# Optimization experiments

Measured on AMD Instinct MI355X. Metric: run time of the kernel, lower is better.

The kernel has to match this reference:

```python
import jax, jax.numpy as jnp
import numpy as np

T, B, D, H = 512, 64, 512, 512  # seq_len, batch, input_size, hidden_size


def setup_inputs() -> dict:
    key = jax.random.key(0)
    ks = jax.random.split(key, 7)
    s = 1.0 / np.sqrt(H)
    return {
        "input": jax.random.normal(ks[0], (T, B, D), dtype=jnp.float32),
        "h0": jax.random.normal(ks[1], (B, H), dtype=jnp.float32),
        "c0": jax.random.normal(ks[2], (B, H), dtype=jnp.float32),
        "W_ih": jax.random.normal(ks[3], (4 * H, D), dtype=jnp.float32) * s,
        "W_hh": jax.random.normal(ks[4], (4 * H, H), dtype=jnp.float32) * s,
        "b_ih": jax.random.normal(ks[5], (4 * H,), dtype=jnp.float32) * s,
        "b_hh": jax.random.normal(ks[6], (4 * H,), dtype=jnp.float32) * s,
        "batch_first": 0,
    }


def reference(input, h0, c0, W_ih, W_hh, b_ih, b_hh, batch_first):
    # Dense (non-packed) branch of RNNLayer.forward with an LSTM cell.
    x = jnp.swapaxes(input, 0, 1) if batch_first else input  # [T, B, D]
    # Input projection is independent of the recurrence: precompute for all t.
    x_proj = jnp.einsum('tbd,gd->tbg', x, W_ih) + b_ih  # [T, B, 4H]

    def step(carry, xt):
        h, c = carry
        gates = xt + h @ W_hh.T + b_hh  # [B, 4H]
        i, f, g, o = jnp.split(gates, 4, axis=-1)
        c_new = jax.nn.sigmoid(f) * c + jax.nn.sigmoid(i) * jnp.tanh(g)
        h_new = jax.nn.sigmoid(o) * jnp.tanh(c_new)
        return (h_new, c_new), h_new

    (hT, cT), ys = jax.lax.scan(step, (h0, c0), x_proj)  # ys: [T, B, H]
    outputs = jnp.swapaxes(ys, 0, 1) if batch_first else ys
    return outputs, hT, cT
```

## Files before the change

### kernel.cpp

```cpp
#include <hip/hip_runtime.h>

typedef __attribute__((ext_vector_type(8))) short bfrag;
typedef __attribute__((ext_vector_type(4))) float f32x4;
typedef __attribute__((ext_vector_type(4))) int i32x4;

#define NT 512
#define NB 64
#define KD 512
#define NG 2048
#define GB 4
#define GH 16

#define YS_SZ (NT * NB * KD)
#define HT_OFF YS_SZ
#define CT_OFF (YS_SZ + NB * KD)

#define MB_BLK_WORDS 4096
#define MB_PAR_WORDS (GB * MB_BLK_WORDS)
#define MB_BYTES (2 * MB_PAR_WORDS * 8)

__device__ __forceinline__ unsigned short f2bf(float f) {
  unsigned u = __float_as_uint(f);
  u += 0x7fffu + ((u >> 16) & 1u);
  return (unsigned short)(u >> 16);
}
__device__ __forceinline__ float bf2f(unsigned short h) {
  return __uint_as_float(((unsigned)h) << 16);
}
__device__ __forceinline__ float sigm(float v) { return 1.f / (1.f + __expf(-v)); }
__device__ __forceinline__ float tanh_f(float v) { return 1.f - 2.f / (__expf(2.f * v) + 1.f); }

__global__ __launch_bounds__(256) void cvt_bf16(const float* __restrict__ src,
                                                unsigned short* __restrict__ dst, int n8) {
  int i = blockIdx.x * 256 + threadIdx.x;
  if (i >= n8) return;
  const float4 a = *(const float4*)(src + (size_t)i * 8);
  const float4 b = *(const float4*)(src + (size_t)i * 8 + 4);
  i32x4 v;
  v.x = (int)(f2bf(a.x) | ((unsigned)f2bf(a.y) << 16));
  v.y = (int)(f2bf(a.z) | ((unsigned)f2bf(a.w) << 16));
  v.z = (int)(f2bf(b.x) | ((unsigned)f2bf(b.y) << 16));
  v.w = (int)(f2bf(b.z) | ((unsigned)f2bf(b.w) << 16));
  *(i32x4*)(dst + (size_t)i * 8) = v;
}
// ... 20 lines not shown
    *(i32x4*)&Xt[srow * 40 + schunk] = *(const i32x4*)(Xb + (m0 + srow) * KD + kb + schunk);
    __syncthreads();
    bfrag af = *(const bfrag*)&Wt[(wid * 16 + cc) * 40 + g * 8];
#pragma unroll
    for (int mt = 0; mt < 4; ++mt) {
      bfrag bf = *(const bfrag*)&Xt[(mt * 16 + cc) * 40 + g * 8];
      acc[mt] = __builtin_amdgcn_mfma_f32_16x16x32_bf16(af, bf, acc[mt], 0, 0, 0);
    }
  }
  const int nl = wid * 16 + g * 4;
  float bi[4];
#pragma unroll
  for (int r = 0; r < 4; ++r) bi[r] = bias[n0 + nl + r];
#pragma unroll
  for (int mt = 0; mt < 4; ++mt) {
#pragma unroll
    for (int r = 0; r < 4; ++r) {
      float v = acc[mt][r] + bi[r];
      size_t idx = ((size_t)t * NG + n0 + nl + r) * 64 + mt * 16 + cc;
      if (XP32) ((float*)XPv)[idx] = v;
      else ((unsigned short*)XPv)[idx] = f2bf(v);
    }
  }
}

template <int XP32>
__global__ __launch_bounds__(256, 1) void lstm_rec(const unsigned short* __restrict__ Whh,
                                                   const void* __restrict__ XPv,
                                                   const float* __restrict__ bhh,
                                                   const float* __restrict__ h0,
                                                   const float* __restrict__ c0,
                                                   unsigned long long* __restrict__ mbox,
                                                   float* __restrict__ out) {
  __shared__ unsigned short hl[16 * 512];

  const int tid = threadIdx.x;
  const int lane = tid & 63, wid = tid >> 6;
  const int g = lane >> 4, cc = lane & 15;
  const int blk = blockIdx.x >> 4, slice = blockIdx.x & 15;
  const int b0 = blk * 16, d0 = slice * 32;

  {
    const int lp = tid >> 4, b = tid & 15;
    const int d = d0 + lp * 2;
    const float* hp = h0 + (size_t)(b0 + b) * KD + d;
    unsigned d32 = (unsigned)f2bf(hp[0]) | ((unsigned)f2bf(hp[1]) << 16);
    __hip_atomic_store(mbox + (size_t)blk * MB_BLK_WORDS + ((d0 >> 1) + lp) * 16 + b,
                       (1ull << 32) | (unsigned long long)d32, __ATOMIC_RELAXED,
                       __HIP_MEMORY_SCOPE_AGENT);
  }

  bfrag w[2][16];
#pragma unroll
  for (int j = 0; j < 2; ++j) {
    const int tt = wid * 2 + j;
    const int r = tt * 16 + cc;
    const size_t n = (size_t)(r & 3) * KD + d0 + (r >> 2);
#pragma unroll
    for (int ks = 0; ks < 16; ++ks)
      w[j][ks] = *(const bfrag*)(Whh + n * KD + ks * 32 + g * 8);
  }
  float bh[2][4], creg[2];
#pragma unroll
  for (int j = 0; j < 2; ++j) {
    const int d = d0 + (wid * 2 + j) * 4 + g;
#pragma unroll
    for (int r = 0; r < 4; ++r) bh[j][r] = bhh[r * KD + d];
    creg[j] = c0[(b0 + cc) * KD + d];
  }

  unsigned long long q0, q1, q2, q3, q4, q5, q6, q7, q8, q9, q10, q11, q12, q13, q14, q15;

#define PISSUE(MB, r)                                                       \
  asm volatile("global_load_dwordx2 %0, %1, %2 sc1"                         \
               : "=v"(q##r)                                                 \
               : "v"((unsigned)(tid * 8 + r * 2048)), "s"(MB) : "memory")
#define PISSUE_ALL(MB)                                                      \
  do {                                                                      \
    PISSUE(MB, 0); PISSUE(MB, 1); PISSUE(MB, 2); PISSUE(MB, 3);             \
    PISSUE(MB, 4); PISSUE(MB, 5); PISSUE(MB, 6); PISSUE(MB, 7);             \
    PISSUE(MB, 8); PISSUE(MB, 9); PISSUE(MB, 10); PISSUE(MB, 11);           \
    PISSUE(MB, 12); PISSUE(MB, 13); PISSUE(MB, 14); PISSUE(MB, 15);         \
  } while (0)
#define PCHK_ALL(okv, tg)                                                   \
  do {                                                                      \
    okv = 1u;                                                               \
    okv &= ((unsigned)(q0 >> 32) == (tg)); okv &= ((unsigned)(q1 >> 32) == (tg));   \
    okv &= ((unsigned)(q2 >> 32) == (tg)); okv &= ((unsigned)(q3 >> 32) == (tg));   \
    okv &= ((unsigned)(q4 >> 32) == (tg)); okv &= ((unsigned)(q5 >> 32) == (tg));   \
    okv &= ((unsigned)(q6 >> 32) == (tg)); okv &= ((unsigned)(q7 >> 32) == (tg));   \
    okv &= ((unsigned)(q8 >> 32) == (tg)); okv &= ((unsigned)(q9 >> 32) == (tg));   \
    okv &= ((unsigned)(q10 >> 32) == (tg)); okv &= ((unsigned)(q11 >> 32) == (tg)); \
    okv &= ((unsigned)(q12 >> 32) == (tg)); okv &= ((unsigned)(q13 >> 32) == (tg)); \
    okv &= ((unsigned)(q14 >> 32) == (tg)); okv &= ((unsigned)(q15 >> 32) == (tg)); \
  } while (0)

  {
    const unsigned long long* nb = mbox + (size_t)blk * MB_BLK_WORDS;
    PISSUE_ALL(nb);
  }

  for (int t = 0; t < NT; ++t) {
    unsigned xpr[2][4];
#pragma unroll
    for (int j = 0; j < 2; ++j) {
      const int d = d0 + (wid * 2 + j) * 4 + g;
#pragma unroll
      for (int r = 0; r < 4; ++r) {
        const size_t idx = ((size_t)t * NG + r * KD + d) * 64 + b0 + cc;
        if constexpr (XP32) {
          const float* p = (const float*)XPv + idx;
          asm volatile("global_load_dword %0, %1, off" : "=v"(xpr[j][r]) : "v"(p) : "memory");
        } else {
          const unsigned short* p = (const unsigned short*)XPv + idx;
          asm volatile("global_load_ushort %0, %1, off" : "=v"(xpr[j][r]) : "v"(p) : "memory");
        }
      }
    }
    const unsigned long long* mbr =
        mbox + (size_t)(t & 1) * MB_PAR_WORDS + (size_t)blk * MB_BLK_WORDS;
    const unsigned tg = (unsigned)(t + 1);
    asm volatile("s_waitcnt vmcnt(8)" ::: "memory");
    __builtin_amdgcn_sched_barrier(0);
    unsigned ok;
    PCHK_ALL(ok, tg);
    while (!__all(ok)) {
      PISSUE_ALL(mbr);
      asm volatile("s_waitcnt vmcnt(0)" ::: "memory");
      __builtin_amdgcn_sched_barrier(0);
      PCHK_ALL(ok, tg);
    }
    {
      const int b = tid & 15, pq = tid >> 4;
      const int bb = b * 1024, bx = (b & 7) << 4;
#define PUNP(r) \
  *(unsigned*)((char*)hl + bb + (((r * 16 + pq) * 4) ^ bx)) = (unsigned)q##r;
      PUNP(0) PUNP(1) PUNP(2) PUNP(3) PUNP(4) PUNP(5) PUNP(6) PUNP(7)
      PUNP(8) PUNP(9) PUNP(10) PUNP(11) PUNP(12) PUNP(13) PUNP(14) PUNP(15)
#undef PUNP
    }
    __syncthreads();
    f32x4 p00 = {0.f, 0.f, 0.f, 0.f}, p01 = {0.f, 0.f, 0.f, 0.f};
    f32x4 p10 = {0.f, 0.f, 0.f, 0.f}, p11 = {0.f, 0.f, 0.f, 0.f};
#pragma unroll
    for (int ks = 0; ks < 8; ++ks) {
      const int off = ks * 64 + g * 16;
      bfrag hb = *(const bfrag*)((const char*)hl + cc * 1024 + (off ^ ((cc & 7) << 4)));
      p00 = __builtin_amdgcn_mfma_f32_16x16x32_bf16(w[0][ks], hb, p00, 0, 0, 0);
      p10 = __builtin_amdgcn_mfma_f32_16x16x32_bf16(w[1][ks], hb, p10, 0, 0, 0);
    }
#pragma unroll
    for (int ks = 8; ks < 16; ++ks) {
      const int off = ks * 64 + g * 16;
      bfrag hb = *(const bfrag*)((const char*)hl + cc * 1024 + (off ^ ((cc & 7) << 4)));
      p01 = __builtin_amdgcn_mfma_f32_16x16x32_bf16(w[0][ks], hb, p01, 0, 0, 0);
      p11 = __builtin_amdgcn_mfma_f32_16x16x32_bf16(w[1][ks], hb, p11, 0, 0, 0);
    }
    const f32x4 acc0 = p00 + p01, acc1 = p10 + p11;
    asm volatile("s_waitcnt vmcnt(0)" ::: "memory");
    __builtin_amdgcn_sched_barrier(0);
    float hnv[2];
#pragma unroll
    for (int j = 0; j < 2; ++j) {
      const f32x4 a = j ? acc1 : acc0;
      float x0, x1, x2, x3;
      if constexpr (XP32) {
        x0 = __uint_as_float(xpr[j][0]); x1 = __uint_as_float(xpr[j][1]);
        x2 = __uint_as_float(xpr[j][2]); x3 = __uint_as_float(xpr[j][3]);
      } else {
        x0 = bf2f((unsigned short)xpr[j][0]); x1 = bf2f((unsigned short)xpr[j][1]);
        x2 = bf2f((unsigned short)xpr[j][2]); x3 = bf2f((unsigned short)xpr[j][3]);
      }
      float gi = a[0] + x0 + bh[j][0];
      float gf = a[1] + x1 + bh[j][1];
      float gg = a[2] + x2 + bh[j][2];
      float go = a[3] + x3 + bh[j][3];
      float cn = sigm(gf) * creg[j] + sigm(gi) * tanh_f(gg);
      creg[j] = cn;
      hnv[j] = sigm(go) * tanh_f(cn);
    }
    {
      unsigned long long* mbw =
          mbox + (size_t)((t + 1) & 1) * MB_PAR_WORDS + (size_t)blk * MB_BLK_WORDS;
      const unsigned long long tagn = (unsigned long long)(unsigned)(t + 2) << 32;
      const float o0 = __shfl_xor(hnv[0], 16);
      const float o1 = __shfl_xor(hnv[1], 16);
      if (!(g & 1)) {
        const unsigned w0 = (unsigned)f2bf(hnv[0]) | ((unsigned)f2bf(o0) << 16);
        const unsigned w1 = (unsigned)f2bf(hnv[1]) | ((unsigned)f2bf(o1) << 16);
        const int p0 = (d0 >> 1) + wid * 4 + (g >> 1);
        const int p1 = p0 + 2;
        __hip_atomic_store(mbw + p0 * 16 + cc, tagn | (unsigned long long)w0,
                           __ATOMIC_RELAXED, __HIP_MEMORY_SCOPE_AGENT);
        __hip_atomic_store(mbw + p1 * 16 + cc, tagn | (unsigned long long)w1,
                           __ATOMIC_RELAXED, __HIP_MEMORY_SCOPE_AGENT);
      }
    }
    {
      float* yb = out + (size_t)t * NB * KD + (size_t)(b0 + cc) * KD + d0 + wid * 8 + g;
      yb[0] = hnv[0];
      yb[4] = hnv[1];
      if (t == NT - 1) {
        float* hb = out + HT_OFF + (size_t)(b0 + cc) * KD + d0 + wid * 8 + g;
        hb[0] = hnv[0];
        hb[4] = hnv[1];
        float* cb = out + CT_OFF + (size_t)(b0 + cc) * KD + d0 + wid * 8 + g;
        cb[0] = creg[0];
        cb[4] = creg[1];
      }
    }
    {
      const unsigned long long* nb =
          mbox + (size_t)((t + 1) & 1) * MB_PAR_WORDS + (size_t)blk * MB_BLK_WORDS;
      PISSUE_ALL(nb);
    }
  }
#undef PISSUE
#undef PISSUE_ALL
#undef PCHK_ALL
}

extern "C" void kernel_launch(void* const* d_in, const int* in_sizes, int n_in,
                              void* d_out, int out_size, void* d_ws, size_t ws_size,
                              hipStream_t stream) {
  const float* x = (const float*)d_in[0];
  const float* h0 = (const float*)d_in[1];
  const float* c0 = (const float*)d_in[2];
  const float* Wih = (const float*)d_in[3];
  const float* Whh = (const float*)d_in[4];
  const float* bih = (const float*)d_in[5];
  const float* bhh = (const float*)d_in[6];
  float* out = (float*)d_out;
  char* ws = (char*)d_ws;

  unsigned long long* mbox = (unsigned long long*)ws;
  unsigned short* WhhB = (unsigned short*)(ws + MB_BYTES);
  unsigned short* WihB = (unsigned short*)(ws + MB_BYTES + 2097152);
  unsigned short* XB = (unsigned short*)(ws + MB_BYTES + 2 * 2097152);
  const size_t xp_off = MB_BYTES + 2ull * 2097152 + 33554432;
  void* XP = (void*)(ws + xp_off);
  const bool xp32 = ws_size >= xp_off + (size_t)NT * NG * 64 * 4;

  hipMemsetAsync(ws, 0, MB_BYTES, stream);

  const int nx8 = NT * NB * KD / 8;
  const int nw8 = NG * KD / 8;
  cvt_bf16<<<dim3(nx8 / 256), 256, 0, stream>>>(x, XB, nx8);
  cvt_bf16<<<dim3(nw8 / 256), 256, 0, stream>>>(Wih, WihB, nw8);
  cvt_bf16<<<dim3(nw8 / 256), 256, 0, stream>>>(Whh, WhhB, nw8);

  if (xp32) {
    xproj_gemm<1><<<dim3(NG / 64, NT), 256, 0, stream>>>(WihB, XB, bih, XP);
    lstm_rec<1><<<dim3(GB * GH), 256, 0, stream>>>(WhhB, XP, bhh, h0, c0, mbox, out);
  } else {
    xproj_gemm<0><<<dim3(NG / 64, NT), 256, 0, stream>>>(WihB, XB, bih, XP);
    lstm_rec<0><<<dim3(GB * GH), 256, 0, stream>>>(WhhB, XP, bhh, h0, c0, mbox, out);
  }
}
```

Measured before the change: 1.486 ms.

## Prefetch next-step input projection, double-buffer LDS h, retry only stale mailbox slots

The input-projection loads for step t+1 are now issued after the mailbox poll for step t succeeds, so they overlap the MFMA and gate work. The h tile in LDS is double-buffered by step parity. The mailbox poll now re-issues only the slots whose tag is stale, instead of reloading all sixteen. The early prefetch of the next mailbox at the end of each step is removed, so the first poll now happens only at the top of the next step and may see more stale slots and retries.

```diff
diff --git a/kernel.cpp b/kernel.cpp
--- a/kernel.cpp
+++ b/kernel.cpp
@@ -96,7 +96,7 @@
                                                    const float* __restrict__ c0,
                                                    unsigned long long* __restrict__ mbox,
                                                    float* __restrict__ out) {
-  __shared__ unsigned short hl[16 * 512];
+  __shared__ unsigned short hl[2][16 * 512];
 
   const int tid = threadIdx.x;
   const int lane = tid & 63, wid = tid >> 6;
@@ -134,11 +134,30 @@
   }
 
   unsigned long long q0, q1, q2, q3, q4, q5, q6, q7, q8, q9, q10, q11, q12, q13, q14, q15;
+  unsigned xp_cur[2][4], xp_nxt[2][4];
+
+  auto xp_issue = [&](unsigned(&dst)[2][4], int tt) {
+#pragma unroll
+    for (int j = 0; j < 2; ++j) {
+      const int d = d0 + (wid * 2 + j) * 4 + g;
+#pragma unroll
+      for (int r = 0; r < 4; ++r) {
+        const size_t idx = ((size_t)tt * NG + r * KD + d) * 64 + b0 + cc;
+        if constexpr (XP32) {
+          const float* p = (const float*)XPv + idx;
+          asm volatile("global_load_dword %0, %1, off" : "=v"(dst[j][r]) : "v"(p) : "memory");
+        } else {
+          const unsigned short* p = (const unsigned short*)XPv + idx;
+          asm volatile("global_load_ushort %0, %1, off" : "=v"(dst[j][r]) : "v"(p) : "memory");
+        }
+      }
+    }
+  };
 
 #define PISSUE(MB, r)                                                       \
   asm volatile("global_load_dwordx2 %0, %1, %2 sc1"                         \
                : "=v"(q##r)                                                 \
-               : "v"((unsigned)(tid * 8 + r * 2048)), "s"(MB) : "memory")
+               : "v"((unsigned)(tid * 8 + (r) * 2048)), "s"(MB) : "memory")
 #define PISSUE_ALL(MB)                                                      \
   do {                                                                      \
     PISSUE(MB, 0); PISSUE(MB, 1); PISSUE(MB, 2); PISSUE(MB, 3);             \
@@ -146,94 +165,87 @@
     PISSUE(MB, 8); PISSUE(MB, 9); PISSUE(MB, 10); PISSUE(MB, 11);           \
     PISSUE(MB, 12); PISSUE(MB, 13); PISSUE(MB, 14); PISSUE(MB, 15);         \
   } while (0)
-#define PCHK_ALL(okv, tg)                                                   \
+#define PMSK1(ms, tg, r) ms |= ((unsigned)(q##r >> 32) != (tg)) ? (1u << (r)) : 0u;
+#define PMSK_ALL(ms, tg)                                                    \
   do {                                                                      \
-    okv = 1u;                                                               \
-    okv &= ((unsigned)(q0 >> 32) == (tg)); okv &= ((unsigned)(q1 >> 32) == (tg));   \
-    okv &= ((unsigned)(q2 >> 32) == (tg)); okv &= ((unsigned)(q3 >> 32) == (tg));   \
-    okv &= ((unsigned)(q4 >> 32) == (tg)); okv &= ((unsigned)(q5 >> 32) == (tg));   \
-    okv &= ((unsigned)(q6 >> 32) == (tg)); okv &= ((unsigned)(q7 >> 32) == (tg));   \
-    okv &= ((unsigned)(q8 >> 32) == (tg)); okv &= ((unsigned)(q9 >> 32) == (tg));   \
-    okv &= ((unsigned)(q10 >> 32) == (tg)); okv &= ((unsigned)(q11 >> 32) == (tg)); \
-    okv &= ((unsigned)(q12 >> 32) == (tg)); okv &= ((unsigned)(q13 >> 32) == (tg)); \
-    okv &= ((unsigned)(q14 >> 32) == (tg)); okv &= ((unsigned)(q15 >> 32) == (tg)); \
+    ms = 0u;                                                                \
+    PMSK1(ms, tg, 0) PMSK1(ms, tg, 1) PMSK1(ms, tg, 2) PMSK1(ms, tg, 3)     \
+    PMSK1(ms, tg, 4) PMSK1(ms, tg, 5) PMSK1(ms, tg, 6) PMSK1(ms, tg, 7)     \
+    PMSK1(ms, tg, 8) PMSK1(ms, tg, 9) PMSK1(ms, tg, 10) PMSK1(ms, tg, 11)   \
+    PMSK1(ms, tg, 12) PMSK1(ms, tg, 13) PMSK1(ms, tg, 14) PMSK1(ms, tg, 15) \
   } while (0)
-
-  {
-    const unsigned long long* nb = mbox + (size_t)blk * MB_BLK_WORDS;
-    PISSUE_ALL(nb);
-  }
+#define PRET1(ms, MB, r) if (__any((ms) & (1u << (r)))) PISSUE(MB, r);
+#define PRET_ALL(ms, MB)                                                    \
+  do {                                                                      \
+    PRET1(ms, MB, 0) PRET1(ms, MB, 1) PRET1(ms, MB, 2) PRET1(ms, MB, 3)     \
+    PRET1(ms, MB, 4) PRET1(ms, MB, 5) PRET1(ms, MB, 6) PRET1(ms, MB, 7)     \
+    PRET1(ms, MB, 8) PRET1(ms, MB, 9) PRET1(ms, MB, 10) PRET1(ms, MB, 11)   \
+    PRET1(ms, MB, 12) PRET1(ms, MB, 13) PRET1(ms, MB, 14) PRET1(ms, MB, 15) \
+  } while (0)
+
+  xp_issue(xp_nxt, 0);
 
   for (int t = 0; t < NT; ++t) {
-    unsigned xpr[2][4];
-#pragma unroll
-    for (int j = 0; j < 2; ++j) {
-      const int d = d0 + (wid * 2 + j) * 4 + g;
-#pragma unroll
-      for (int r = 0; r < 4; ++r) {
-        const size_t idx = ((size_t)t * NG + r * KD + d) * 64 + b0 + cc;
-        if constexpr (XP32) {
-          const float* p = (const float*)XPv + idx;
-          asm volatile("global_load_dword %0, %1, off" : "=v"(xpr[j][r]) : "v"(p) : "memory");
-        } else {
-          const unsigned short* p = (const unsigned short*)XPv + idx;
-          asm volatile("global_load_ushort %0, %1, off" : "=v"(xpr[j][r]) : "v"(p) : "memory");
-        }
-      }
-    }
+    const int par = t & 1;
     const unsigned long long* mbr =
-        mbox + (size_t)(t & 1) * MB_PAR_WORDS + (size_t)blk * MB_BLK_WORDS;
+        mbox + (size_t)par * MB_PAR_WORDS + (size_t)blk * MB_BLK_WORDS;
     const unsigned tg = (unsigned)(t + 1);
-    asm volatile("s_waitcnt vmcnt(8)" ::: "memory");
+    PISSUE_ALL(mbr);
+    asm volatile("s_waitcnt vmcnt(0)" ::: "memory");
     __builtin_amdgcn_sched_barrier(0);
-    unsigned ok;
-    PCHK_ALL(ok, tg);
-    while (!__all(ok)) {
-      PISSUE_ALL(mbr);
+#pragma unroll
+    for (int j = 0; j < 2; ++j)
+#pragma unroll
+      for (int r = 0; r < 4; ++r) xp_cur[j][r] = xp_nxt[j][r];
+    unsigned ms;
+    PMSK_ALL(ms, tg);
+    while (__any(ms != 0u)) {
+      PRET_ALL(ms, mbr);
       asm volatile("s_waitcnt vmcnt(0)" ::: "memory");
       __builtin_amdgcn_sched_barrier(0);
-      PCHK_ALL(ok, tg);
-    }
+      PMSK_ALL(ms, tg);
+    }
+    xp_issue(xp_nxt, (t + 1 < NT) ? t + 1 : t);
     {
+      char* hlb = (char*)&hl[par][0];
       const int b = tid & 15, pq = tid >> 4;
       const int bb = b * 1024, bx = (b & 7) << 4;
-#define PUNP(r) \
-  *(unsigned*)((char*)hl + bb + (((r * 16 + pq) * 4) ^ bx)) = (unsigned)q##r;
+#define PUNP(r) *(unsigned*)(hlb + bb + ((((r)*16 + pq) * 4) ^ bx)) = (unsigned)q##r;
       PUNP(0) PUNP(1) PUNP(2) PUNP(3) PUNP(4) PUNP(5) PUNP(6) PUNP(7)
       PUNP(8) PUNP(9) PUNP(10) PUNP(11) PUNP(12) PUNP(13) PUNP(14) PUNP(15)
 #undef PUNP
     }
     __syncthreads();
+    const char* hrb = (const char*)&hl[par][0] + cc * 1024;
+    const int cx = (cc & 7) << 4;
     f32x4 p00 = {0.f, 0.f, 0.f, 0.f}, p01 = {0.f, 0.f, 0.f, 0.f};
     f32x4 p10 = {0.f, 0.f, 0.f, 0.f}, p11 = {0.f, 0.f, 0.f, 0.f};
 #pragma unroll
     for (int ks = 0; ks < 8; ++ks) {
       const int off = ks * 64 + g * 16;
-      bfrag hb = *(const bfrag*)((const char*)hl + cc * 1024 + (off ^ ((cc & 7) << 4)));
+      bfrag hb = *(const bfrag*)(hrb + (off ^ cx));
       p00 = __builtin_amdgcn_mfma_f32_16x16x32_bf16(w[0][ks], hb, p00, 0, 0, 0);
       p10 = __builtin_amdgcn_mfma_f32_16x16x32_bf16(w[1][ks], hb, p10, 0, 0, 0);
     }
 #pragma unroll
     for (int ks = 8; ks < 16; ++ks) {
       const int off = ks * 64 + g * 16;
-      bfrag hb = *(const bfrag*)((const char*)hl + cc * 1024 + (off ^ ((cc & 7) << 4)));
+      bfrag hb = *(const bfrag*)(hrb + (off ^ cx));
       p01 = __builtin_amdgcn_mfma_f32_16x16x32_bf16(w[0][ks], hb, p01, 0, 0, 0);
       p11 = __builtin_amdgcn_mfma_f32_16x16x32_bf16(w[1][ks], hb, p11, 0, 0, 0);
     }
     const f32x4 acc0 = p00 + p01, acc1 = p10 + p11;
-    asm volatile("s_waitcnt vmcnt(0)" ::: "memory");
-    __builtin_amdgcn_sched_barrier(0);
     float hnv[2];
 #pragma unroll
     for (int j = 0; j < 2; ++j) {
       const f32x4 a = j ? acc1 : acc0;
       float x0, x1, x2, x3;
       if constexpr (XP32) {
-        x0 = __uint_as_float(xpr[j][0]); x1 = __uint_as_float(xpr[j][1]);
-        x2 = __uint_as_float(xpr[j][2]); x3 = __uint_as_float(xpr[j][3]);
+        x0 = __uint_as_float(xp_cur[j][0]); x1 = __uint_as_float(xp_cur[j][1]);
+        x2 = __uint_as_float(xp_cur[j][2]); x3 = __uint_as_float(xp_cur[j][3]);
       } else {
-        x0 = bf2f((unsigned short)xpr[j][0]); x1 = bf2f((unsigned short)xpr[j][1]);
-        x2 = bf2f((unsigned short)xpr[j][2]); x3 = bf2f((unsigned short)xpr[j][3]);
+        x0 = bf2f((unsigned short)xp_cur[j][0]); x1 = bf2f((unsigned short)xp_cur[j][1]);
+        x2 = bf2f((unsigned short)xp_cur[j][2]); x3 = bf2f((unsigned short)xp_cur[j][3]);
       }
       float gi = a[0] + x0 + bh[j][0];
       float gf = a[1] + x1 + bh[j][1];
@@ -273,15 +285,13 @@
         cb[4] = creg[1];
       }
     }
-    {
-      const unsigned long long* nb =
-          mbox + (size_t)((t + 1) & 1) * MB_PAR_WORDS + (size_t)blk * MB_BLK_WORDS;
-      PISSUE_ALL(nb);
-    }
   }
 #undef PISSUE
 #undef PISSUE_ALL
-#undef PCHK_ALL
+#undef PMSK1
+#undef PMSK_ALL
+#undef PRET1
+#undef PRET_ALL
 }
 
 extern "C" void kernel_launch(void* const* d_in, const int* in_sizes, int n_in,
```

Result: no change. 1.461 ms (-1.7%).

## Process two batch groups per workgroup, halving recurrent grid size

Applied to the files above, without the earlier changes.

Each workgroup of the recurrent kernel now handles two 16-row batch groups for the same hidden slice, running them one after the other inside each time step. The W_hh slice held in registers is reused across both groups, and the grid shrinks from 64 to 32 workgroups. The mailbox prefetch that used to be issued after each step is dropped, so every group polls the mailbox synchronously. The two groups are serialised within a step, which lengthens the per-step critical path and removes the overlap between the mailbox read and other work.

```diff
diff --git a/kernel.cpp b/kernel.cpp
--- a/kernel.cpp
+++ b/kernel.cpp
@@ -96,15 +96,17 @@
                                                    const float* __restrict__ c0,
                                                    unsigned long long* __restrict__ mbox,
                                                    float* __restrict__ out) {
-  __shared__ unsigned short hl[16 * 512];
+  __shared__ unsigned short hl[2][16 * 512];
 
   const int tid = threadIdx.x;
   const int lane = tid & 63, wid = tid >> 6;
   const int g = lane >> 4, cc = lane & 15;
-  const int blk = blockIdx.x >> 4, slice = blockIdx.x & 15;
-  const int b0 = blk * 16, d0 = slice * 32;
-
-  {
+  const int slice = blockIdx.x & 15, pair = blockIdx.x >> 4;
+  const int d0 = slice * 32;
+
+#pragma unroll
+  for (int cix = 0; cix < 2; ++cix) {
+    const int blk = pair * 2 + cix, b0 = blk * 16;
     const int lp = tid >> 4, b = tid & 15;
     const int d = d0 + lp * 2;
     const float* hp = h0 + (size_t)(b0 + b) * KD + d;
@@ -124,13 +126,20 @@
     for (int ks = 0; ks < 16; ++ks)
       w[j][ks] = *(const bfrag*)(Whh + n * KD + ks * 32 + g * 8);
   }
-  float bh[2][4], creg[2];
+  float bh[2][4];
 #pragma unroll
   for (int j = 0; j < 2; ++j) {
     const int d = d0 + (wid * 2 + j) * 4 + g;
 #pragma unroll
     for (int r = 0; r < 4; ++r) bh[j][r] = bhh[r * KD + d];
-    creg[j] = c0[(b0 + cc) * KD + d];
+  }
+  float creg[2][2];
+#pragma unroll
+  for (int cix = 0; cix < 2; ++cix) {
+    const int b0 = (pair * 2 + cix) * 16;
+#pragma unroll
+    for (int j = 0; j < 2; ++j)
+      creg[cix][j] = c0[(size_t)(b0 + cc) * KD + d0 + (wid * 2 + j) * 4 + g];
   }
 
   unsigned long long q0, q1, q2, q3, q4, q5, q6, q7, q8, q9, q10, q11, q12, q13, q14, q15;
@@ -138,7 +147,7 @@
 #define PISSUE(MB, r)                                                       \
   asm volatile("global_load_dwordx2 %0, %1, %2 sc1"                         \
                : "=v"(q##r)                                                 \
-               : "v"((unsigned)(tid * 8 + r * 2048)), "s"(MB) : "memory")
+               : "v"((unsigned)(tid * 8 + (r) * 2048)), "s"(MB) : "memory")
 #define PISSUE_ALL(MB)                                                      \
   do {                                                                      \
     PISSUE(MB, 0); PISSUE(MB, 1); PISSUE(MB, 2); PISSUE(MB, 3);             \
@@ -159,124 +168,117 @@
     okv &= ((unsigned)(q14 >> 32) == (tg)); okv &= ((unsigned)(q15 >> 32) == (tg)); \
   } while (0)
 
-  {
-    const unsigned long long* nb = mbox + (size_t)blk * MB_BLK_WORDS;
-    PISSUE_ALL(nb);
-  }
-
   for (int t = 0; t < NT; ++t) {
-    unsigned xpr[2][4];
-#pragma unroll
-    for (int j = 0; j < 2; ++j) {
-      const int d = d0 + (wid * 2 + j) * 4 + g;
-#pragma unroll
-      for (int r = 0; r < 4; ++r) {
-        const size_t idx = ((size_t)t * NG + r * KD + d) * 64 + b0 + cc;
+    const int par = t & 1;
+    const unsigned tg = (unsigned)(t + 1);
+    const unsigned long long tagn = (unsigned long long)(unsigned)(t + 2) << 32;
+#pragma unroll
+    for (int cix = 0; cix < 2; ++cix) {
+      const int blk = pair * 2 + cix, b0 = blk * 16;
+      unsigned xpr[2][4];
+#pragma unroll
+      for (int j = 0; j < 2; ++j) {
+        const int d = d0 + (wid * 2 + j) * 4 + g;
+#pragma unroll
+        for (int r = 0; r < 4; ++r) {
+          const size_t idx = ((size_t)t * NG + r * KD + d) * 64 + b0 + cc;
+          if constexpr (XP32) {
+            const float* p = (const float*)XPv + idx;
+            asm volatile("global_load_dword %0, %1, off" : "=v"(xpr[j][r]) : "v"(p) : "memory");
+          } else {
+            const unsigned short* p = (const unsigned short*)XPv + idx;
+            asm volatile("global_load_ushort %0, %1, off" : "=v"(xpr[j][r]) : "v"(p) : "memory");
+          }
+        }
+      }
+      const unsigned long long* mbr =
+          mbox + (size_t)par * MB_PAR_WORDS + (size_t)blk * MB_BLK_WORDS;
+      unsigned ok;
+      for (;;) {
+        PISSUE_ALL(mbr);
+        asm volatile("s_waitcnt vmcnt(0)" ::: "memory");
+        __builtin_amdgcn_sched_barrier(0);
+        PCHK_ALL(ok, tg);
+        if (__all(ok)) break;
+      }
+      {
+        char* hlb = (char*)&hl[cix][0];
+        const int b = tid & 15, pq = tid >> 4;
+        const int bb = b * 1024, bx = (b & 7) << 4;
+#define PUNP(r) *(unsigned*)(hlb + bb + ((((r)*16 + pq) * 4) ^ bx)) = (unsigned)q##r;
+        PUNP(0) PUNP(1) PUNP(2) PUNP(3) PUNP(4) PUNP(5) PUNP(6) PUNP(7)
+        PUNP(8) PUNP(9) PUNP(10) PUNP(11) PUNP(12) PUNP(13) PUNP(14) PUNP(15)
+#undef PUNP
+      }
+      __syncthreads();
+      const char* hrb = (const char*)&hl[cix][0] + cc * 1024;
+      const int cx = (cc & 7) << 4;
+      f32x4 p00 = {0.f, 0.f, 0.f, 0.f}, p01 = {0.f, 0.f, 0.f, 0.f};
+      f32x4 p10 = {0.f, 0.f, 0.f, 0.f}, p11 = {0.f, 0.f, 0.f, 0.f};
+#pragma unroll
+      for (int ks = 0; ks < 8; ++ks) {
+        const int off = ks * 64 + g * 16;
+        bfrag hb = *(const bfrag*)(hrb + (off ^ cx));
+        p00 = __builtin_amdgcn_mfma_f32_16x16x32_bf16(w[0][ks], hb, p00, 0, 0, 0);
+        p10 = __builtin_amdgcn_mfma_f32_16x16x32_bf16(w[1][ks], hb, p10, 0, 0, 0);
+      }
+#pragma unroll
+      for (int ks = 8; ks < 16; ++ks) {
+        const int off = ks * 64 + g * 16;
+        bfrag hb = *(const bfrag*)(hrb + (off ^ cx));
+        p01 = __builtin_amdgcn_mfma_f32_16x16x32_bf16(w[0][ks], hb, p01, 0, 0, 0);
+        p11 = __builtin_amdgcn_mfma_f32_16x16x32_bf16(w[1][ks], hb, p11, 0, 0, 0);
+      }
+      const f32x4 acc0 = p00 + p01, acc1 = p10 + p11;
+      float hnv[2];
+#pragma unroll
+      for (int j = 0; j < 2; ++j) {
+        const f32x4 a = j ? acc1 : acc0;
+        float x0, x1, x2, x3;
         if constexpr (XP32) {
-          const float* p = (const float*)XPv + idx;
-          asm volatile("global_load_dword %0, %1, off" : "=v"(xpr[j][r]) : "v"(p) : "memory");
+          x0 = __uint_as_float(xpr[j][0]); x1 = __uint_as_float(xpr[j][1]);
+          x2 = __uint_as_float(xpr[j][2]); x3 = __uint_as_float(xpr[j][3]);
         } else {
-          const unsigned short* p = (const unsigned short*)XPv + idx;
-          asm volatile("global_load_ushort %0, %1, off" : "=v"(xpr[j][r]) : "v"(p) : "memory");
+          x0 = bf2f((unsigned short)xpr[j][0]); x1 = bf2f((unsigned short)xpr[j][1]);
+          x2 = bf2f((unsigned short)xpr[j][2]); x3 = bf2f((unsigned short)xpr[j][3]);
         }
-      }
-    }
-    const unsigned long long* mbr =
-        mbox + (size_t)(t & 1) * MB_PAR_WORDS + (size_t)blk * MB_BLK_WORDS;
-    const unsigned tg = (unsigned)(t + 1);
-    asm volatile("s_waitcnt vmcnt(8)" ::: "memory");
-    __builtin_amdgcn_sched_barrier(0);
-    unsigned ok;
-    PCHK_ALL(ok, tg);
-    while (!__all(ok)) {
-      PISSUE_ALL(mbr);
-      asm volatile("s_waitcnt vmcnt(0)" ::: "memory");
-      __builtin_amdgcn_sched_barrier(0);
-      PCHK_ALL(ok, tg);
-    }
-    {
-      const int b = tid & 15, pq = tid >> 4;
-      const int bb = b * 1024, bx = (b & 7) << 4;
-#define PUNP(r) \
-  *(unsigned*)((char*)hl + bb + (((r * 16 + pq) * 4) ^ bx)) = (unsigned)q##r;
-      PUNP(0) PUNP(1) PUNP(2) PUNP(3) PUNP(4) PUNP(5) PUNP(6) PUNP(7)
-      PUNP(8) PUNP(9) PUNP(10) PUNP(11) PUNP(12) PUNP(13) PUNP(14) PUNP(15)
-#undef PUNP
-    }
-    __syncthreads();
-    f32x4 p00 = {0.f, 0.f, 0.f, 0.f}, p01 = {0.f, 0.f, 0.f, 0.f};
-    f32x4 p10 = {0.f, 0.f, 0.f, 0.f}, p11 = {0.f, 0.f, 0.f, 0.f};
-#pragma unroll
-    for (int ks = 0; ks < 8; ++ks) {
-      const int off = ks * 64 + g * 16;
-      bfrag hb = *(const bfrag*)((const char*)hl + cc * 1024 + (off ^ ((cc & 7) << 4)));
-      p00 = __builtin_amdgcn_mfma_f32_16x16x32_bf16(w[0][ks], hb, p00, 0, 0, 0);
-      p10 = __builtin_amdgcn_mfma_f32_16x16x32_bf16(w[1][ks], hb, p10, 0, 0, 0);
-    }
-#pragma unroll
-    for (int ks = 8; ks < 16; ++ks) {
-      const int off = ks * 64 + g * 16;
-      bfrag hb = *(const bfrag*)((const char*)hl + cc * 1024 + (off ^ ((cc & 7) << 4)));
-      p01 = __builtin_amdgcn_mfma_f32_16x16x32_bf16(w[0][ks], hb, p01, 0, 0, 0);
-      p11 = __builtin_amdgcn_mfma_f32_16x16x32_bf16(w[1][ks], hb, p11, 0, 0, 0);
-    }
-    const f32x4 acc0 = p00 + p01, acc1 = p10 + p11;
-    asm volatile("s_waitcnt vmcnt(0)" ::: "memory");
-    __builtin_amdgcn_sched_barrier(0);
-    float hnv[2];
-#pragma unroll
-    for (int j = 0; j < 2; ++j) {
-      const f32x4 a = j ? acc1 : acc0;
-      float x0, x1, x2, x3;
-      if constexpr (XP32) {
-        x0 = __uint_as_float(xpr[j][0]); x1 = __uint_as_float(xpr[j][1]);
-        x2 = __uint_as_float(xpr[j][2]); x3 = __uint_as_float(xpr[j][3]);
-      } else {
-        x0 = bf2f((unsigned short)xpr[j][0]); x1 = bf2f((unsigned short)xpr[j][1]);
-        x2 = bf2f((unsigned short)xpr[j][2]); x3 = bf2f((unsigned short)xpr[j][3]);
-      }
-      float gi = a[0] + x0 + bh[j][0];
-      float gf = a[1] + x1 + bh[j][1];
-      float gg = a[2] + x2 + bh[j][2];
-      float go = a[3] + x3 + bh[j][3];
-      float cn = sigm(gf) * creg[j] + sigm(gi) * tanh_f(gg);
-      creg[j] = cn;
-      hnv[j] = sigm(go) * tanh_f(cn);
-    }
-    {
-      unsigned long long* mbw =
-          mbox + (size_t)((t + 1) & 1) * MB_PAR_WORDS + (size_t)blk * MB_BLK_WORDS;
-      const unsigned long long tagn = (unsigned long long)(unsigned)(t + 2) << 32;
-      const float o0 = __shfl_xor(hnv[0], 16);
-      const float o1 = __shfl_xor(hnv[1], 16);
-      if (!(g & 1)) {
-        const unsigned w0 = (unsigned)f2bf(hnv[0]) | ((unsigned)f2bf(o0) << 16);
-        const unsigned w1 = (unsigned)f2bf(hnv[1]) | ((unsigned)f2bf(o1) << 16);
-        const int p0 = (d0 >> 1) + wid * 4 + (g >> 1);
-        const int p1 = p0 + 2;
-        __hip_atomic_store(mbw + p0 * 16 + cc, tagn | (unsigned long long)w0,
-                           __ATOMIC_RELAXED, __HIP_MEMORY_SCOPE_AGENT);
-        __hip_atomic_store(mbw + p1 * 16 + cc, tagn | (unsigned long long)w1,
-                           __ATOMIC_RELAXED, __HIP_MEMORY_SCOPE_AGENT);
-      }
-    }
-    {
-      float* yb = out + (size_t)t * NB * KD + (size_t)(b0 + cc) * KD + d0 + wid * 8 + g;
-      yb[0] = hnv[0];
-      yb[4] = hnv[1];
-      if (t == NT - 1) {
-        float* hb = out + HT_OFF + (size_t)(b0 + cc) * KD + d0 + wid * 8 + g;
-        hb[0] = hnv[0];
-        hb[4] = hnv[1];
-        float* cb = out + CT_OFF + (size_t)(b0 + cc) * KD + d0 + wid * 8 + g;
-        cb[0] = creg[0];
-        cb[4] = creg[1];
-      }
-    }
-    {
-      const unsigned long long* nb =
-          mbox + (size_t)((t + 1) & 1) * MB_PAR_WORDS + (size_t)blk * MB_BLK_WORDS;
-      PISSUE_ALL(nb);
+        float gi = a[0] + x0 + bh[j][0];
+        float gf = a[1] + x1 + bh[j][1];
+        float gg = a[2] + x2 + bh[j][2];
+        float go = a[3] + x3 + bh[j][3];
+        float cn = sigm(gf) * creg[cix][j] + sigm(gi) * tanh_f(gg);
+        creg[cix][j] = cn;
+        hnv[j] = sigm(go) * tanh_f(cn);
+      }
+      {
+        unsigned long long* mbw =
+            mbox + (size_t)(par ^ 1) * MB_PAR_WORDS + (size_t)blk * MB_BLK_WORDS;
+        const float o0 = __shfl_xor(hnv[0], 16);
+        const float o1 = __shfl_xor(hnv[1], 16);
+        if (!(g & 1)) {
+          const unsigned w0 = (unsigned)f2bf(hnv[0]) | ((unsigned)f2bf(o0) << 16);
+          const unsigned w1 = (unsigned)f2bf(hnv[1]) | ((unsigned)f2bf(o1) << 16);
+          const int p0 = (d0 >> 1) + wid * 4 + (g >> 1);
+          const int p1 = p0 + 2;
+          __hip_atomic_store(mbw + p0 * 16 + cc, tagn | (unsigned long long)w0,
+                             __ATOMIC_RELAXED, __HIP_MEMORY_SCOPE_AGENT);
+          __hip_atomic_store(mbw + p1 * 16 + cc, tagn | (unsigned long long)w1,
+                             __ATOMIC_RELAXED, __HIP_MEMORY_SCOPE_AGENT);
+        }
+      }
+      {
+        float* yb = out + (size_t)t * NB * KD + (size_t)(b0 + cc) * KD + d0 + wid * 8 + g;
+        yb[0] = hnv[0];
+        yb[4] = hnv[1];
+        if (t == NT - 1) {
+          float* hb = out + HT_OFF + (size_t)(b0 + cc) * KD + d0 + wid * 8 + g;
+          hb[0] = hnv[0];
+          hb[4] = hnv[1];
+          float* cb = out + CT_OFF + (size_t)(b0 + cc) * KD + d0 + wid * 8 + g;
+          cb[0] = creg[cix][0];
+          cb[4] = creg[cix][1];
+        }
+      }
     }
   }
 #undef PISSUE
@@ -315,9 +317,9 @@
 
   if (xp32) {
     xproj_gemm<1><<<dim3(NG / 64, NT), 256, 0, stream>>>(WihB, XB, bih, XP);
-    lstm_rec<1><<<dim3(GB * GH), 256, 0, stream>>>(WhhB, XP, bhh, h0, c0, mbox, out);
+    lstm_rec<1><<<dim3(GB * GH / 2), 256, 0, stream>>>(WhhB, XP, bhh, h0, c0, mbox, out);
   } else {
     xproj_gemm<0><<<dim3(NG / 64, NT), 256, 0, stream>>>(WihB, XB, bih, XP);
-    lstm_rec<0><<<dim3(GB * GH), 256, 0, stream>>>(WhhB, XP, bhh, h0, c0, mbox, out);
-  }
-}
+    lstm_rec<0><<<dim3(GB * GH / 2), 256, 0, stream>>>(WhhB, XP, bhh, h0, c0, mbox, out);
+  }
+}
```

Result: slower. 2.567 ms (+72.7%).

## Process two batch groups per block to overlap mailbox polling with compute

Applied to the files above, without the earlier changes.

Each recurrence block now handles two 16-row batch groups (A and B) for its hidden-dim slice, which halves the grid from 64 to 32 blocks. While group A's matrix-multiply and gate math run, the block polls group B's mailbox, and the reverse, so cross-block synchronization latency is hidden behind the other group's work. The W_hh fragments are loaded once and reused for both groups, and each group gets its own LDS buffer. In exchange, each block does twice the serial work per timestep and only half as many CUs are used.

```diff
diff --git a/kernel.cpp b/kernel.cpp
--- a/kernel.cpp
+++ b/kernel.cpp
@@ -9,7 +9,6 @@
 #define KD 512
 #define NG 2048
 #define GB 4
-#define GH 16
 
 #define YS_SZ (NT * NB * KD)
 #define HT_OFF YS_SZ
@@ -96,15 +95,20 @@
                                                    const float* __restrict__ c0,
                                                    unsigned long long* __restrict__ mbox,
                                                    float* __restrict__ out) {
-  __shared__ unsigned short hl[16 * 512];
+  __shared__ unsigned short hl0[16 * 512];
+  __shared__ unsigned short hl1[16 * 512];
 
   const int tid = threadIdx.x;
   const int lane = tid & 63, wid = tid >> 6;
   const int g = lane >> 4, cc = lane & 15;
-  const int blk = blockIdx.x >> 4, slice = blockIdx.x & 15;
-  const int b0 = blk * 16, d0 = slice * 32;
-
-  {
+  const int slice = blockIdx.x & 15, pair = blockIdx.x >> 4;
+  const int d0 = slice * 32;
+  const int blkA = pair * 2, blkB = pair * 2 + 1;
+  const int b0A = blkA * 16, b0B = blkB * 16;
+
+#pragma unroll
+  for (int cix = 0; cix < 2; ++cix) {
+    const int blk = cix ? blkB : blkA, b0 = blk * 16;
     const int lp = tid >> 4, b = tid & 15;
     const int d = d0 + lp * 2;
     const float* hp = h0 + (size_t)(b0 + b) * KD + d;
@@ -124,21 +128,24 @@
     for (int ks = 0; ks < 16; ++ks)
       w[j][ks] = *(const bfrag*)(Whh + n * KD + ks * 32 + g * 8);
   }
-  float bh[2][4], creg[2];
+  float bh[2][4];
 #pragma unroll
   for (int j = 0; j < 2; ++j) {
     const int d = d0 + (wid * 2 + j) * 4 + g;
 #pragma unroll
     for (int r = 0; r < 4; ++r) bh[j][r] = bhh[r * KD + d];
-    creg[j] = c0[(b0 + cc) * KD + d];
-  }
+  }
+  float cregA0 = c0[(size_t)(b0A + cc) * KD + d0 + wid * 8 + g];
+  float cregA1 = c0[(size_t)(b0A + cc) * KD + d0 + wid * 8 + 4 + g];
+  float cregB0 = c0[(size_t)(b0B + cc) * KD + d0 + wid * 8 + g];
+  float cregB1 = c0[(size_t)(b0B + cc) * KD + d0 + wid * 8 + 4 + g];
 
   unsigned long long q0, q1, q2, q3, q4, q5, q6, q7, q8, q9, q10, q11, q12, q13, q14, q15;
 
 #define PISSUE(MB, r)                                                       \
   asm volatile("global_load_dwordx2 %0, %1, %2 sc1"                         \
                : "=v"(q##r)                                                 \
-               : "v"((unsigned)(tid * 8 + r * 2048)), "s"(MB) : "memory")
+               : "v"((unsigned)(tid * 8 + (r) * 2048)), "s"(MB) : "memory")
 #define PISSUE_ALL(MB)                                                      \
   do {                                                                      \
     PISSUE(MB, 0); PISSUE(MB, 1); PISSUE(MB, 2); PISSUE(MB, 3);             \
@@ -158,130 +165,214 @@
     okv &= ((unsigned)(q12 >> 32) == (tg)); okv &= ((unsigned)(q13 >> 32) == (tg)); \
     okv &= ((unsigned)(q14 >> 32) == (tg)); okv &= ((unsigned)(q15 >> 32) == (tg)); \
   } while (0)
+#define PUNPACK(HLB)                                                        \
+  do {                                                                      \
+    char* hlb_ = (char*)(HLB);                                              \
+    const int b_ = tid & 15, pq_ = tid >> 4;                                \
+    const int bb_ = b_ * 1024, bx_ = (b_ & 7) << 4;                         \
+    *(unsigned*)(hlb_ + bb_ + (((0 * 16 + pq_) * 4) ^ bx_)) = (unsigned)q0;   \
+    *(unsigned*)(hlb_ + bb_ + (((1 * 16 + pq_) * 4) ^ bx_)) = (unsigned)q1;   \
+    *(unsigned*)(hlb_ + bb_ + (((2 * 16 + pq_) * 4) ^ bx_)) = (unsigned)q2;   \
+    *(unsigned*)(hlb_ + bb_ + (((3 * 16 + pq_) * 4) ^ bx_)) = (unsigned)q3;   \
+    *(unsigned*)(hlb_ + bb_ + (((4 * 16 + pq_) * 4) ^ bx_)) = (unsigned)q4;   \
+    *(unsigned*)(hlb_ + bb_ + (((5 * 16 + pq_) * 4) ^ bx_)) = (unsigned)q5;   \
+    *(unsigned*)(hlb_ + bb_ + (((6 * 16 + pq_) * 4) ^ bx_)) = (unsigned)q6;   \
+    *(unsigned*)(hlb_ + bb_ + (((7 * 16 + pq_) * 4) ^ bx_)) = (unsigned)q7;   \
+    *(unsigned*)(hlb_ + bb_ + (((8 * 16 + pq_) * 4) ^ bx_)) = (unsigned)q8;   \
+    *(unsigned*)(hlb_ + bb_ + (((9 * 16 + pq_) * 4) ^ bx_)) = (unsigned)q9;   \
+    *(unsigned*)(hlb_ + bb_ + (((10 * 16 + pq_) * 4) ^ bx_)) = (unsigned)q10; \
+    *(unsigned*)(hlb_ + bb_ + (((11 * 16 + pq_) * 4) ^ bx_)) = (unsigned)q11; \
+    *(unsigned*)(hlb_ + bb_ + (((12 * 16 + pq_) * 4) ^ bx_)) = (unsigned)q12; \
+    *(unsigned*)(hlb_ + bb_ + (((13 * 16 + pq_) * 4) ^ bx_)) = (unsigned)q13; \
+    *(unsigned*)(hlb_ + bb_ + (((14 * 16 + pq_) * 4) ^ bx_)) = (unsigned)q14; \
+    *(unsigned*)(hlb_ + bb_ + (((15 * 16 + pq_) * 4) ^ bx_)) = (unsigned)q15; \
+  } while (0)
+#define XP_ISSUE(DST, T, B0)                                                \
+  do {                                                                      \
+    _Pragma("unroll") for (int j_ = 0; j_ < 2; ++j_) {                      \
+      const int d_ = d0 + (wid * 2 + j_) * 4 + g;                           \
+      _Pragma("unroll") for (int r_ = 0; r_ < 4; ++r_) {                    \
+        const size_t idx_ = ((size_t)(T) * NG + r_ * KD + d_) * 64 + (B0) + cc; \
+        if constexpr (XP32) {                                               \
+          const float* p_ = (const float*)XPv + idx_;                       \
+          asm volatile("global_load_dword %0, %1, off"                      \
+                       : "=v"(DST[j_][r_]) : "v"(p_) : "memory");           \
+        } else {                                                            \
+          const unsigned short* p_ = (const unsigned short*)XPv + idx_;     \
+          asm volatile("global_load_ushort %0, %1, off"                     \
+                       : "=v"(DST[j_][r_]) : "v"(p_) : "memory");           \
+        }                                                                   \
+      }                                                                     \
+    }                                                                       \
+  } while (0)
+#define VMCNT(N) do { asm volatile("s_waitcnt vmcnt(" #N ")" ::: "memory"); \
+                      __builtin_amdgcn_sched_barrier(0); } while (0)
+#define MFMA_BLOCK(HLB, ACC0, ACC1)                                         \
+  do {                                                                      \
+    const char* hrb_ = (const char*)(HLB) + cc * 1024;                      \
+    const int cx_ = (cc & 7) << 4;                                          \
+    f32x4 s00 = {0.f, 0.f, 0.f, 0.f}, s01 = {0.f, 0.f, 0.f, 0.f};           \
+    f32x4 s10 = {0.f, 0.f, 0.f, 0.f}, s11 = {0.f, 0.f, 0.f, 0.f};           \
+    _Pragma("unroll") for (int ks_ = 0; ks_ < 8; ++ks_) {                   \
+      bfrag hb_ = *(const bfrag*)(hrb_ + ((ks_ * 64 + g * 16) ^ cx_));      \
+      s00 = __builtin_amdgcn_mfma_f32_16x16x32_bf16(w[0][ks_], hb_, s00, 0, 0, 0); \
+      s10 = __builtin_amdgcn_mfma_f32_16x16x32_bf16(w[1][ks_], hb_, s10, 0, 0, 0); \
+    }                                                                       \
+    _Pragma("unroll") for (int ks_ = 8; ks_ < 16; ++ks_) {                  \
+      bfrag hb_ = *(const bfrag*)(hrb_ + ((ks_ * 64 + g * 16) ^ cx_));      \
+      s01 = __builtin_amdgcn_mfma_f32_16x16x32_bf16(w[0][ks_], hb_, s01, 0, 0, 0); \
+      s11 = __builtin_amdgcn_mfma_f32_16x16x32_bf16(w[1][ks_], hb_, s11, 0, 0, 0); \
+    }                                                                       \
+    ACC0 = s00 + s01; ACC1 = s10 + s11;                                     \
+  } while (0)
 
   {
-    const unsigned long long* nb = mbox + (size_t)blk * MB_BLK_WORDS;
-    PISSUE_ALL(nb);
-  }
+    const unsigned long long* mbA0 = mbox + (size_t)blkA * MB_BLK_WORDS;
+    PISSUE_ALL(mbA0);
+  }
+
+  unsigned xpA[2][4], xpB[2][4];
 
   for (int t = 0; t < NT; ++t) {
-    unsigned xpr[2][4];
-#pragma unroll
-    for (int j = 0; j < 2; ++j) {
-      const int d = d0 + (wid * 2 + j) * 4 + g;
-#pragma unroll
-      for (int r = 0; r < 4; ++r) {
-        const size_t idx = ((size_t)t * NG + r * KD + d) * 64 + b0 + cc;
-        if constexpr (XP32) {
-          const float* p = (const float*)XPv + idx;
-          asm volatile("global_load_dword %0, %1, off" : "=v"(xpr[j][r]) : "v"(p) : "memory");
-        } else {
-          const unsigned short* p = (const unsigned short*)XPv + idx;
-          asm volatile("global_load_ushort %0, %1, off" : "=v"(xpr[j][r]) : "v"(p) : "memory");
-        }
-      }
-    }
-    const unsigned long long* mbr =
-        mbox + (size_t)(t & 1) * MB_PAR_WORDS + (size_t)blk * MB_BLK_WORDS;
+    const int par = t & 1;
     const unsigned tg = (unsigned)(t + 1);
-    asm volatile("s_waitcnt vmcnt(8)" ::: "memory");
-    __builtin_amdgcn_sched_barrier(0);
+    const unsigned long long tagn = (unsigned long long)(unsigned)(t + 2) << 32;
+    const unsigned long long* mbrA = mbox + (size_t)par * MB_PAR_WORDS + (size_t)blkA * MB_BLK_WORDS;
+    const unsigned long long* mbrB = mbox + (size_t)par * MB_PAR_WORDS + (size_t)blkB * MB_BLK_WORDS;
+    unsigned long long* mbwA = mbox + (size_t)(par ^ 1) * MB_PAR_WORDS + (size_t)blkA * MB_BLK_WORDS;
+    unsigned long long* mbwB = mbox + (size_t)(par ^ 1) * MB_PAR_WORDS + (size_t)blkB * MB_BLK_WORDS;
+
+    XP_ISSUE(xpA, t, b0A);
+    VMCNT(8);
     unsigned ok;
     PCHK_ALL(ok, tg);
     while (!__all(ok)) {
-      PISSUE_ALL(mbr);
-      asm volatile("s_waitcnt vmcnt(0)" ::: "memory");
-      __builtin_amdgcn_sched_barrier(0);
+      PISSUE_ALL(mbrA);
+      VMCNT(0);
       PCHK_ALL(ok, tg);
     }
+    PUNPACK(hl0);
+    __syncthreads();
+    PISSUE_ALL(mbrB);
+    f32x4 accA0, accA1;
+    MFMA_BLOCK(hl0, accA0, accA1);
+    VMCNT(16);
+    float hnA0, hnA1;
     {
-      const int b = tid & 15, pq = tid >> 4;
-      const int bb = b * 1024, bx = (b & 7) << 4;
-#define PUNP(r) \
-  *(unsigned*)((char*)hl + bb + (((r * 16 + pq) * 4) ^ bx)) = (unsigned)q##r;
-      PUNP(0) PUNP(1) PUNP(2) PUNP(3) PUNP(4) PUNP(5) PUNP(6) PUNP(7)
-      PUNP(8) PUNP(9) PUNP(10) PUNP(11) PUNP(12) PUNP(13) PUNP(14) PUNP(15)
-#undef PUNP
-    }
+      float x00, x01, x02, x03, x10, x11, x12, x13;
+      if constexpr (XP32) {
+        x00 = __uint_as_float(xpA[0][0]); x01 = __uint_as_float(xpA[0][1]);
+        x02 = __uint_as_float(xpA[0][2]); x03 = __uint_as_float(xpA[0][3]);
+        x10 = __uint_as_float(xpA[1][0]); x11 = __uint_as_float(xpA[1][1]);
+        x12 = __uint_as_float(xpA[1][2]); x13 = __uint_as_float(xpA[1][3]);
+      } else {
+        x00 = bf2f((unsigned short)xpA[0][0]); x01 = bf2f((unsigned short)xpA[0][1]);
+        x02 = bf2f((unsigned short)xpA[0][2]); x03 = bf2f((unsigned short)xpA[0][3]);
+        x10 = bf2f((unsigned short)xpA[1][0]); x11 = bf2f((unsigned short)xpA[1][1]);
+        x12 = bf2f((unsigned short)xpA[1][2]); x13 = bf2f((unsigned short)xpA[1][3]);
+      }
+      float gi = accA0[0] + x00 + bh[0][0], gf = accA0[1] + x01 + bh[0][1];
+      float gg = accA0[2] + x02 + bh[0][2], go = accA0[3] + x03 + bh[0][3];
+      float cn = sigm(gf) * cregA0 + sigm(gi) * tanh_f(gg);
+      cregA0 = cn; hnA0 = sigm(go) * tanh_f(cn);
+      gi = accA1[0] + x10 + bh[1][0]; gf = accA1[1] + x11 + bh[1][1];
+      gg = accA1[2] + x12 + bh[1][2]; go = accA1[3] + x13 + bh[1][3];
+      cn = sigm(gf) * cregA1 + sigm(gi) * tanh_f(gg);
+      cregA1 = cn; hnA1 = sigm(go) * tanh_f(cn);
+    }
+    {
+      const float o0 = __shfl_xor(hnA0, 16);
+      const float o1 = __shfl_xor(hnA1, 16);
+      if (!(g & 1)) {
+        const unsigned w0 = (unsigned)f2bf(hnA0) | ((unsigned)f2bf(o0) << 16);
+        const unsigned w1 = (unsigned)f2bf(hnA1) | ((unsigned)f2bf(o1) << 16);
+        const int p0 = (d0 >> 1) + wid * 4 + (g >> 1);
+        __hip_atomic_store(mbwA + p0 * 16 + cc, tagn | (unsigned long long)w0,
+                           __ATOMIC_RELAXED, __HIP_MEMORY_SCOPE_AGENT);
+        __hip_atomic_store(mbwA + (p0 + 2) * 16 + cc, tagn | (unsigned long long)w1,
+                           __ATOMIC_RELAXED, __HIP_MEMORY_SCOPE_AGENT);
+      }
+      float* yb = out + (size_t)t * NB * KD + (size_t)(b0A + cc) * KD + d0 + wid * 8 + g;
+      yb[0] = hnA0;
+      yb[4] = hnA1;
+      if (t == NT - 1) {
+        float* hb = out + HT_OFF + (size_t)(b0A + cc) * KD + d0 + wid * 8 + g;
+        hb[0] = hnA0; hb[4] = hnA1;
+        float* cb = out + CT_OFF + (size_t)(b0A + cc) * KD + d0 + wid * 8 + g;
+        cb[0] = cregA0; cb[4] = cregA1;
+      }
+    }
+    XP_ISSUE(xpB, t, b0B);
+    VMCNT(8);
+    PCHK_ALL(ok, tg);
+    while (!__all(ok)) {
+      PISSUE_ALL(mbrB);
+      VMCNT(0);
+      PCHK_ALL(ok, tg);
+    }
+    PUNPACK(hl1);
     __syncthreads();
-    f32x4 p00 = {0.f, 0.f, 0.f, 0.f}, p01 = {0.f, 0.f, 0.f, 0.f};
-    f32x4 p10 = {0.f, 0.f, 0.f, 0.f}, p11 = {0.f, 0.f, 0.f, 0.f};
-#pragma unroll
-    for (int ks = 0; ks < 8; ++ks) {
-      const int off = ks * 64 + g * 16;
-      bfrag hb = *(const bfrag*)((const char*)hl + cc * 1024 + (off ^ ((cc & 7) << 4)));
-      p00 = __builtin_amdgcn_mfma_f32_16x16x32_bf16(w[0][ks], hb, p00, 0, 0, 0);
-      p10 = __builtin_amdgcn_mfma_f32_16x16x32_bf16(w[1][ks], hb, p10, 0, 0, 0);
-    }
-#pragma unroll
-    for (int ks = 8; ks < 16; ++ks) {
-      const int off = ks * 64 + g * 16;
-      bfrag hb = *(const bfrag*)((const char*)hl + cc * 1024 + (off ^ ((cc & 7) << 4)));
-      p01 = __builtin_amdgcn_mfma_f32_16x16x32_bf16(w[0][ks], hb, p01, 0, 0, 0);
-      p11 = __builtin_amdgcn_mfma_f32_16x16x32_bf16(w[1][ks], hb, p11, 0, 0, 0);
-    }
-    const f32x4 acc0 = p00 + p01, acc1 = p10 + p11;
-    asm volatile("s_waitcnt vmcnt(0)" ::: "memory");
-    __builtin_amdgcn_sched_barrier(0);
-    float hnv[2];
-#pragma unroll
-    for (int j = 0; j < 2; ++j) {
-      const f32x4 a = j ? acc1 : acc0;
-      float x0, x1, x2, x3;
+    {
+      const unsigned long long* mbrA1 =
+          mbox + (size_t)(par ^ 1) * MB_PAR_WORDS + (size_t)blkA * MB_BLK_WORDS;
+      PISSUE_ALL(mbrA1);
+    }
+    f32x4 accB0, accB1;
+    MFMA_BLOCK(hl1, accB0, accB1);
+    VMCNT(16);
+    float hnB0, hnB1;
+    {
+      float x00, x01, x02, x03, x10, x11, x12, x13;
       if constexpr (XP32) {
-        x0 = __uint_as_float(xpr[j][0]); x1 = __uint_as_float(xpr[j][1]);
-        x2 = __uint_as_float(xpr[j][2]); x3 = __uint_as_float(xpr[j][3]);
+        x00 = __uint_as_float(xpB[0][0]); x01 = __uint_as_float(xpB[0][1]);
+        x02 = __uint_as_float(xpB[0][2]); x03 = __uint_as_float(xpB[0][3]);
+        x10 = __uint_as_float(xpB[1][0]); x11 = __uint_as_float(xpB[1][1]);
+        x12 = __uint_as_float(xpB[1][2]); x13 = __uint_as_float(xpB[1][3]);
       } else {
-        x0 = bf2f((unsigned short)xpr[j][0]); x1 = bf2f((unsigned short)xpr[j][1]);
-        x2 = bf2f((unsigned short)xpr[j][2]); x3 = bf2f((unsigned short)xpr[j][3]);
-      }
-      float gi = a[0] + x0 + bh[j][0];
-      float gf = a[1] + x1 + bh[j][1];
-      float gg = a[2] + x2 + bh[j][2];
-      float go = a[3] + x3 + bh[j][3];
-      float cn = sigm(gf) * creg[j] + sigm(gi) * tanh_f(gg);
-      creg[j] = cn;
-      hnv[j] = sigm(go) * tanh_f(cn);
+        x00 = bf2f((unsigned short)xpB[0][0]); x01 = bf2f((unsigned short)xpB[0][1]);
+        x02 = bf2f((unsigned short)xpB[0][2]); x03 = bf2f((unsigned short)xpB[0][3]);
+        x10 = bf2f((unsigned short)xpB[1][0]); x11 = bf2f((unsigned short)xpB[1][1]);
+        x12 = bf2f((unsigned short)xpB[1][2]); x13 = bf2f((unsigned short)xpB[1][3]);
+      }
+      float gi = accB0[0] + x00 + bh[0][0], gf = accB0[1] + x01 + bh[0][1];
+      float gg = accB0[2] + x02 + bh[0][2], go = accB0[3] + x03 + bh[0][3];
+      float cn = sigm(gf) * cregB0 + sigm(gi) * tanh_f(gg);
+      cregB0 = cn; hnB0 = sigm(go) * tanh_f(cn);
+      gi = accB1[0] + x10 + bh[1][0]; gf = accB1[1] + x11 + bh[1][1];
+      gg = accB1[2] + x12 + bh[1][2]; go = accB1[3] + x13 + bh[1][3];
+      cn = sigm(gf) * cregB1 + sigm(gi) * tanh_f(gg);
+      cregB1 = cn; hnB1 = sigm(go) * tanh_f(cn);
     }
     {
-      unsigned long long* mbw =
-          mbox + (size_t)((t + 1) & 1) * MB_PAR_WORDS + (size_t)blk * MB_BLK_WORDS;
-      const unsigned long long tagn = (unsigned long long)(unsigned)(t + 2) << 32;
-      const float o0 = __shfl_xor(hnv[0], 16);
-      const float o1 = __shfl_xor(hnv[1], 16);
+      const float o0 = __shfl_xor(hnB0, 16);
+      const float o1 = __shfl_xor(hnB1, 16);
       if (!(g & 1)) {
-        const unsigned w0 = (unsigned)f2bf(hnv[0]) | ((unsigned)f2bf(o0) << 16);
-        const unsigned w1 = (unsigned)f2bf(hnv[1]) | ((unsigned)f2bf(o1) << 16);
+        const unsigned w0 = (unsigned)f2bf(hnB0) | ((unsigned)f2bf(o0) << 16);
+        const unsigned w1 = (unsigned)f2bf(hnB1) | ((unsigned)f2bf(o1) << 16);
         const int p0 = (d0 >> 1) + wid * 4 + (g >> 1);
-        const int p1 = p0 + 2;
-        __hip_atomic_store(mbw + p0 * 16 + cc, tagn | (unsigned long long)w0,
+        __hip_atomic_store(mbwB + p0 * 16 + cc, tagn | (unsigned long long)w0,
                            __ATOMIC_RELAXED, __HIP_MEMORY_SCOPE_AGENT);
-        __hip_atomic_store(mbw + p1 * 16 + cc, tagn | (unsigned long long)w1,
+        __hip_atomic_store(mbwB + (p0 + 2) * 16 + cc, tagn | (unsigned long long)w1,
                            __ATOMIC_RELAXED, __HIP_MEMORY_SCOPE_AGENT);
       }
-    }
-    {
-      float* yb = out + (size_t)t * NB * KD + (size_t)(b0 + cc) * KD + d0 + wid * 8 + g;
-      yb[0] = hnv[0];
-      yb[4] = hnv[1];
+      float* yb = out + (size_t)t * NB * KD + (size_t)(b0B + cc) * KD + d0 + wid * 8 + g;
+      yb[0] = hnB0;
+      yb[4] = hnB1;
       if (t == NT - 1) {
-        float* hb = out + HT_OFF + (size_t)(b0 + cc) * KD + d0 + wid * 8 + g;
-        hb[0] = hnv[0];
-        hb[4] = hnv[1];
-        float* cb = out + CT_OFF + (size_t)(b0 + cc) * KD + d0 + wid * 8 + g;
-        cb[0] = creg[0];
-        cb[4] = creg[1];
-      }
-    }
-    {
-      const unsigned long long* nb =
-          mbox + (size_t)((t + 1) & 1) * MB_PAR_WORDS + (size_t)blk * MB_BLK_WORDS;
-      PISSUE_ALL(nb);
+        float* hb = out + HT_OFF + (size_t)(b0B + cc) * KD + d0 + wid * 8 + g;
+        hb[0] = hnB0; hb[4] = hnB1;
+        float* cb = out + CT_OFF + (size_t)(b0B + cc) * KD + d0 + wid * 8 + g;
+        cb[0] = cregB0; cb[4] = cregB1;
+      }
     }
   }
 #undef PISSUE
 #undef PISSUE_ALL
 #undef PCHK_ALL
+#undef PUNPACK
+#undef XP_ISSUE
+#undef VMCNT
+#undef MFMA_BLOCK
 }
 
 extern "C" void kernel_launch(void* const* d_in, const int* in_sizes, int n_in,
@@ -315,9 +406,9 @@
 
   if (xp32) {
     xproj_gemm<1><<<dim3(NG / 64, NT), 256, 0, stream>>>(WihB, XB, bih, XP);
-    lstm_rec<1><<<dim3(GB * GH), 256, 0, stream>>>(WhhB, XP, bhh, h0, c0, mbox, out);
+    lstm_rec<1><<<dim3(GB * 16 / 2), 256, 0, stream>>>(WhhB, XP, bhh, h0, c0, mbox, out);
   } else {
     xproj_gemm<0><<<dim3(NG / 64, NT), 256, 0, stream>>>(WihB, XB, bih, XP);
-    lstm_rec<0><<<dim3(GB * GH), 256, 0, stream>>>(WhhB, XP, bhh, h0, c0, mbox, out);
-  }
-}
+    lstm_rec<0><<<dim3(GB * 16 / 2), 256, 0, stream>>>(WhhB, XP, bhh, h0, c0, mbox, out);
+  }
+}
```

Result: slower. 2.367 ms (+59.3%).
